# Kernel optimization log

Hardware: AMD Instinct MI355X
Metric: run time of the kernel (lower is better)

The kernel has to match this reference:

```python
import jax, jax.numpy as jnp
import numpy as np

EPS = 1e-6


def setup_inputs() -> dict:
    key = jax.random.key(0)
    k1, k2 = jax.random.split(key)
    B, Lq, Lk, D = 16, 1024, 1024, 512
    query = jax.random.normal(k1, (B, Lq, D), dtype=jnp.float32)
    context = jax.random.normal(k2, (B, Lk, D), dtype=jnp.float32)
    gamma = jnp.ones((D,), dtype=jnp.float32)
    beta = jnp.zeros((D,), dtype=jnp.float32)
    return {"query": query, "context": context, "gamma": gamma, "beta": beta}


def _layer_norm(x, gamma, beta):
    mean = jnp.mean(x, axis=-1, keepdims=True)
    var = jnp.var(x, axis=-1, keepdims=True)
    return gamma * (x - mean) * jax.lax.rsqrt(var + EPS) + beta


def reference(query, context, gamma, beta):
    # query: [B, Lq, D], context: [B, Lk, D]
    D = query.shape[-1]
    scale = 1.0 / np.sqrt(D).astype(np.float32)
    # additive-style tanh-activated scores: [B, Lq, Lk]
    score = jnp.tanh(jnp.einsum('bqd,bkd->bqk', query, context) * scale)
    attn = jax.nn.softmax(score, axis=2)
    # dropout is identity in eval/reference mode
    out = jnp.einsum('bqk,bkd->bqd', attn, context)
    out = _layer_norm(out + query, gamma, beta)
    return out
```

## Files before the change

kernel.cpp:

```cpp
#include <hip/hip_runtime.h>
#include <hip/hip_bf16.h>
#include <cstdint>

#define LQ 1024
#define LK 1024
#define DD 512
#define NB 16
#define QB 64
#define KB 32
#define NT (LK / KB)
#define CSTRIDE 1088
#define CSZ (32 * CSTRIDE)

typedef short bf16x8 __attribute__((ext_vector_type(8)));
typedef float f32x4 __attribute__((ext_vector_type(4)));

__device__ __forceinline__ uint16_t f2bf(float f) {
  uint32_t u = __builtin_bit_cast(uint32_t, f);
  u = (u + 0x7fffu + ((u >> 16) & 1u)) >> 16;
  return (uint16_t)u;
}

__device__ __forceinline__ void load_lds16(const void* g, void* l) {
  __builtin_amdgcn_global_load_lds(
      (const __attribute__((address_space(1))) uint32_t*)g,
      (__attribute__((address_space(3))) uint32_t*)l, 16, 0, 0);
}

__global__ __launch_bounds__(256) void prep_kernel(const float* __restrict__ c,
                                                   uint16_t* __restrict__ cb,
                                                   uint16_t* __restrict__ ct) {
  __shared__ float t[32][33];
  const int k0 = blockIdx.x * 32, d0 = blockIdx.y * 32, b = blockIdx.z;
  const float* src = c + (size_t)b * LK * DD;
  uint16_t* cbd = cb + (size_t)b * LK * DD;
  uint16_t* ctd = ct + (size_t)b * DD * LK;
  const int tx = threadIdx.x, ty = threadIdx.y;
  for (int j = 0; j < 4; ++j) {
    int k = ty + j * 8;
    float v = src[(size_t)(k0 + k) * DD + d0 + tx];
    t[k][tx] = v;
    cbd[(size_t)(k0 + k) * DD + d0 + tx] = f2bf(v);
  }
  __syncthreads();
  for (int j = 0; j < 4; ++j) {
    int d = ty + j * 8;
    ctd[(size_t)(d0 + d) * LK + k0 + tx] = f2bf(t[tx][d]);
  }
}

__global__ __launch_bounds__(512, 2) void attn_kernel(
    const uint16_t* __restrict__ Cb, const uint16_t* __restrict__ Ctb,
    const float* __restrict__ Qf, const float* __restrict__ gamma,
    const float* __restrict__ beta, float* __restrict__ out) {
  __shared__ uint4 cs4[2 * CSZ / 16];
  __shared__ uint4 cts4[2 * 32 * 1024 / 16];
  __shared__ char plds[64 * 80];
  __shared__ float denom_s[QB];
  __shared__ float rsum_s[QB], rsumsq_s[QB], mean_s[QB], rstd_s[QB];

  const int tid = threadIdx.x;
  const int w = tid >> 6, l = tid & 63, c = l & 15, g = l >> 4;
  const int orig = blockIdx.x;
  const int virt = ((orig & 7) << 5) | (orig >> 3);
  const int b = virt >> 4, qblk = virt & 15;
  const int q0 = qblk * QB;
  const int mt = w & 1, qt = w >> 1;
  const float scale = 0.044194173824159216f;

  if (tid < QB) { denom_s[tid] = 0.f; rsum_s[tid] = 0.f; rsumsq_s[tid] = 0.f; }

  bf16x8 qfrag[16];
  {
    const float* qrow = Qf + ((size_t)b * LQ + q0 + qt * 16 + c) * DD;
    for (int s = 0; s < 16; ++s) {
      float4 a0 = *(const float4*)(qrow + s * 32 + g * 8);
      float4 a1 = *(const float4*)(qrow + s * 32 + g * 8 + 4);
      ushort4 u0, u1;
      u0.x = f2bf(a0.x); u0.y = f2bf(a0.y); u0.z = f2bf(a0.z); u0.w = f2bf(a0.w);
      u1.x = f2bf(a1.x); u1.y = f2bf(a1.y); u1.z = f2bf(a1.z); u1.w = f2bf(a1.w);
      union { ushort4 u[2]; bf16x8 v; } pk;
      pk.u[0] = u0; pk.u[1] = u1;
      qfrag[s] = pk.v;
    }
  }

  const int kkA = mt * 16 + c;
  const int aoff = kkA * CSTRIDE + ((g ^ (kkA & 3)) * 16);

  f32x4 oacc[4][4];
  for (int i = 0; i < 4; ++i)
    for (int j = 0; j < 4; ++j) oacc[i][j] = (f32x4){0.f, 0.f, 0.f, 0.f};
  float dacc = 0.f;

  const char* cbyte = (const char*)Cb + (size_t)b * LK * DD * 2;
  const char* ctbyte = (const char*)Ctb + (size_t)b * DD * LK * 2;

  int csrcoff[4];
  for (int j = 0; j < 4; ++j) {
    int r = w * 4 + j;
    csrcoff[j] = r * 1024 + ((l * 16) ^ ((r & 3) << 4));
  }

  char* cs0 = (char*)cs4;
  char* cs1 = cs0 + CSZ;
  char* cts0 = (char*)cts4;
  char* cts1 = cts0 + 32 * 1024;
  const int pwoff = (qt * 16 + c) * 80 + (mt * 16 + g * 4) * 2;
  const int proff = c * 80 + g * 16;

  auto stageC = [&](char* dst, int kt2) {
    const char* s0 = cbyte + (size_t)kt2 * 32768;
    for (int j = 0; j < 4; ++j)
      load_lds16(s0 + csrcoff[j], dst + (w * 4 + j) * CSTRIDE);
  };
  auto stageCT = [&](char* dst, int kt2) {
    const int kk0 = kt2 * KB;
    for (int j = 0; j < 4; ++j) {
      int d0l = w * 64 + j * 16;
      int d = d0l + (l >> 2);
      const char* src =
          ctbyte + (size_t)d * 2048 + kk0 * 2 + (((l & 3) * 16) ^ ((d & 3) << 4));
      load_lds16(src, dst + d0l * 64);
    }
  };

  stageC(cs0, 0);
  stageCT(cts0, 0);
  __syncthreads();

  for (int kt = 0; kt < NT; ++kt) {
    const int cur = kt & 1;
    const char* csR = cur ? cs1 : cs0;
    const char* ctsR = cur ? cts1 : cts0;
    if (kt + 1 < NT) {
      stageC(cur ? cs0 : cs1, kt + 1);
      stageCT(cur ? cts0 : cts1, kt + 1);
    }
    f32x4 s0v = {0.f, 0.f, 0.f, 0.f}, s1v = {0.f, 0.f, 0.f, 0.f};
    f32x4 s2v = {0.f, 0.f, 0.f, 0.f}, s3v = {0.f, 0.f, 0.f, 0.f};
    {
      const char* ar = csR + aoff;
      for (int s = 0; s < 4; ++s) {
        bf16x8 a0 = *(const bf16x8*)(ar + s * 64);
        bf16x8 a1 = *(const bf16x8*)(ar + (s + 4) * 64);
        bf16x8 a2 = *(const bf16x8*)(ar + (s + 8) * 64);
        bf16x8 a3 = *(const bf16x8*)(ar + (s + 12) * 64);
        s0v = __builtin_amdgcn_mfma_f32_16x16x32_bf16(a0, qfrag[s], s0v, 0, 0, 0);
        s1v = __builtin_amdgcn_mfma_f32_16x16x32_bf16(a1, qfrag[s + 4], s1v, 0, 0, 0);
        s2v = __builtin_amdgcn_mfma_f32_16x16x32_bf16(a2, qfrag[s + 8], s2v, 0, 0, 0);
        s3v = __builtin_amdgcn_mfma_f32_16x16x32_bf16(a3, qfrag[s + 12], s3v, 0, 0, 0);
      }
    }
    {
      float pv[4];
      for (int i = 0; i < 4; ++i) {
        float sv = ((s0v[i] + s1v[i]) + (s2v[i] + s3v[i])) * scale;
        float e2 = __expf(sv * 2.f);
        float r = __builtin_amdgcn_rcpf(e2 + 1.f);
        float th = (e2 - 1.f) * r;
        float p = __expf(th);
        pv[i] = p;
        dacc += p;
      }
      uint2 pk;
      asm("v_cvt_pk_bf16_f32 %0, %1, %2" : "=v"(pk.x) : "v"(pv[0]), "v"(pv[1]));
      asm("v_cvt_pk_bf16_f32 %0, %1, %2" : "=v"(pk.y) : "v"(pv[2]), "v"(pv[3]));
      *(uint2*)(plds + pwoff) = pk;
    }
    asm volatile("s_waitcnt lgkmcnt(0)" ::: "memory");
    __builtin_amdgcn_s_barrier();
    __builtin_amdgcn_sched_barrier(0);

    {
      bf16x8 pa[4], pb[4];
      for (int q2 = 0; q2 < 4; ++q2)
        pa[q2] = *(const bf16x8*)(plds + proff + q2 * 1280);
      for (int nt = 0; nt < 4; ++nt) {
        int d = w * 64 + nt * 16 + c;
        pb[nt] = *(const bf16x8*)(ctsR + d * 64 + ((g * 16) ^ ((d & 3) << 4)));
      }
      for (int q2 = 0; q2 < 4; ++q2)
        for (int n2 = 0; n2 < 4; ++n2)
          oacc[q2][n2] =
              __builtin_amdgcn_mfma_f32_16x16x32_bf16(pa[q2], pb[n2], oacc[q2][n2], 0, 0, 0);
    }
    __syncthreads();
  }

  float dv = dacc;
  dv += __shfl_xor(dv, 16);
  dv += __shfl_xor(dv, 32);
  if (l < 16) atomicAdd(&denom_s[qt * 16 + l], dv);
  __syncthreads();

  const float* qsrc = Qf + ((size_t)b * LQ + q0) * DD;
  for (int q2 = 0; q2 < 4; ++q2)
    for (int i = 0; i < 4; ++i) {
      int row = q2 * 16 + g * 4 + i;
      float inv = 1.f / denom_s[row];
      for (int nt = 0; nt < 4; ++nt) {
        int d = w * 64 + nt * 16 + c;
        float o = oacc[q2][nt][i] * inv + qsrc[(size_t)row * DD + d];
        oacc[q2][nt][i] = o;
      }
    }
  for (int q2 = 0; q2 < 4; ++q2)
    for (int i = 0; i < 4; ++i) {
      float s1 = 0.f, s2 = 0.f;
      for (int nt = 0; nt < 4; ++nt) {
        float v = oacc[q2][nt][i];
        s1 += v;
        s2 += v * v;
      }
      s1 += __shfl_xor(s1, 1); s2 += __shfl_xor(s2, 1);
      s1 += __shfl_xor(s1, 2); s2 += __shfl_xor(s2, 2);
      s1 += __shfl_xor(s1, 4); s2 += __shfl_xor(s2, 4);
      s1 += __shfl_xor(s1, 8); s2 += __shfl_xor(s2, 8);
      if (c == 0) {
        int row = q2 * 16 + g * 4 + i;
        atomicAdd(&rsum_s[row], s1);
        atomicAdd(&rsumsq_s[row], s2);
      }
    }
  __syncthreads();
  if (tid < QB) {
    float m = rsum_s[tid] * (1.f / DD);
    float var = rsumsq_s[tid] * (1.f / DD) - m * m;
    mean_s[tid] = m;
    rstd_s[tid] = rsqrtf(fmaxf(var, 0.f) + 1e-6f);
  }
  __syncthreads();
  float* op = out + ((size_t)b * LQ + q0) * DD;
  for (int q2 = 0; q2 < 4; ++q2)
    for (int i = 0; i < 4; ++i) {
      int row = q2 * 16 + g * 4 + i;
      float m = mean_s[row], r = rstd_s[row];
      for (int nt = 0; nt < 4; ++nt) {
        int d = w * 64 + nt * 16 + c;
        op[(size_t)row * DD + d] = gamma[d] * ((oacc[q2][nt][i] - m) * r) + beta[d];
      }
    }
}

__global__ __launch_bounds__(256) void naive_kernel(const float* __restrict__ Q,
                                                    const float* __restrict__ C,
                                                    const float* __restrict__ gamma,
                                                    const float* __restrict__ beta,
                                                    float* __restrict__ out) {
  const int row = blockIdx.x;
  const int b = row >> 10;
  const int tid = threadIdx.x;
  __shared__ float qs[DD];
  __shared__ float ps[LK];
  __shared__ float ys[DD];
  __shared__ float red[256];
  const float* qp = Q + (size_t)row * DD;
  const float* cb = C + (size_t)b * LK * DD;
  for (int d = tid; d < DD; d += 256) qs[d] = qp[d];
  __syncthreads();
  for (int k = tid; k < LK; k += 256) {
    const float* cr = cb + (size_t)k * DD;
    float s = 0.f;
    for (int d = 0; d < DD; ++d) s += qs[d] * cr[d];
    s *= 0.044194173824159216f;
    float e2 = __expf(2.f * s);
    float th = (e2 - 1.f) / (e2 + 1.f);
    ps[k] = __expf(th);
  }
  __syncthreads();
  float dsum = 0.f;
  for (int k = tid; k < LK; k += 256) dsum += ps[k];
  red[tid] = dsum;
  __syncthreads();
  for (int off = 128; off; off >>= 1) {
    if (tid < off) red[tid] += red[tid + off];
    __syncthreads();
  }
  float inv = 1.f / red[0];
  __syncthreads();
  for (int d = tid; d < DD; d += 256) {
    float o = 0.f;
    for (int k = 0; k < LK; ++k) o += ps[k] * cb[(size_t)k * DD + d];
    ys[d] = o * inv + qs[d];
  }
  __syncthreads();
  float s1 = 0.f;
  for (int d = tid; d < DD; d += 256) s1 += ys[d];
  red[tid] = s1;
  __syncthreads();
  for (int off = 128; off; off >>= 1) {
    if (tid < off) red[tid] += red[tid + off];
    __syncthreads();
  }
  float mean = red[0] * (1.f / DD);
  __syncthreads();
  float s2 = 0.f;
  for (int d = tid; d < DD; d += 256) {
    float v = ys[d] - mean;
    s2 += v * v;
  }
  red[tid] = s2;
  __syncthreads();
  for (int off = 128; off; off >>= 1) {
    if (tid < off) red[tid] += red[tid + off];
    __syncthreads();
  }
  float rstd = rsqrtf(red[0] * (1.f / DD) + 1e-6f);
  for (int d = tid; d < DD; d += 256)
    out[(size_t)row * DD + d] = gamma[d] * ((ys[d] - mean) * rstd) + beta[d];
}

extern "C" void kernel_launch(void* const* d_in, const int* in_sizes, int n_in,
                              void* d_out, int out_size, void* d_ws, size_t ws_size,
                              hipStream_t stream) {
  const float* Qf = (const float*)d_in[0];
  const float* Cf = (const float*)d_in[1];
  const float* gamma = (const float*)d_in[2];
  const float* beta = (const float*)d_in[3];
  float* out = (float*)d_out;
  const size_t nelem = (size_t)NB * LK * DD;
  const size_t need = nelem * 2 * 2;
  if (ws_size >= need) {
    uint16_t* Cb = (uint16_t*)d_ws;
    uint16_t* Ctb = Cb + nelem;
    prep_kernel<<<dim3(LK / 32, DD / 32, NB), dim3(32, 8), 0, stream>>>(Cf, Cb, Ctb);
    attn_kernel<<<256, 512, 0, stream>>>(Cb, Ctb, Qf, gamma, beta, out);
  } else {
    naive_kernel<<<NB * LQ, 256, 0, stream>>>(Qf, Cf, gamma, beta, out);
  }
}
```

Measured before the change: 82.32 us.

## Split waves into score producers and PV consumers with warp specialization

Waves 0-3 now compute the QK scores and tanh-softmax numerators for two query tiles each and write them to shared memory. Waves 4-7 each hold a 64x128 output accumulator and run the P·V MFMAs plus the residual add and layernorm. Each group stages only its own operand (C for the producers, C transposed for the consumers). The aim is to overlap the two GEMM phases across wave groups and to cut redundant staging. The cost is higher register pressure in the consumer waves and lockstep barrier matching between the two branches.

```diff
diff --git a/kernel.cpp b/kernel.cpp
--- a/kernel.cpp
+++ b/kernel.cpp
@@ -65,182 +65,226 @@
   const int virt = ((orig & 7) << 5) | (orig >> 3);
   const int b = virt >> 4, qblk = virt & 15;
   const int q0 = qblk * QB;
-  const int mt = w & 1, qt = w >> 1;
   const float scale = 0.044194173824159216f;
 
   if (tid < QB) { denom_s[tid] = 0.f; rsum_s[tid] = 0.f; rsumsq_s[tid] = 0.f; }
-
-  bf16x8 qfrag[16];
-  {
-    const float* qrow = Qf + ((size_t)b * LQ + q0 + qt * 16 + c) * DD;
-    for (int s = 0; s < 16; ++s) {
-      float4 a0 = *(const float4*)(qrow + s * 32 + g * 8);
-      float4 a1 = *(const float4*)(qrow + s * 32 + g * 8 + 4);
-      ushort4 u0, u1;
-      u0.x = f2bf(a0.x); u0.y = f2bf(a0.y); u0.z = f2bf(a0.z); u0.w = f2bf(a0.w);
-      u1.x = f2bf(a1.x); u1.y = f2bf(a1.y); u1.z = f2bf(a1.z); u1.w = f2bf(a1.w);
-      union { ushort4 u[2]; bf16x8 v; } pk;
-      pk.u[0] = u0; pk.u[1] = u1;
-      qfrag[s] = pk.v;
-    }
-  }
-
-  const int kkA = mt * 16 + c;
-  const int aoff = kkA * CSTRIDE + ((g ^ (kkA & 3)) * 16);
-
-  f32x4 oacc[4][4];
-  for (int i = 0; i < 4; ++i)
-    for (int j = 0; j < 4; ++j) oacc[i][j] = (f32x4){0.f, 0.f, 0.f, 0.f};
-  float dacc = 0.f;
 
   const char* cbyte = (const char*)Cb + (size_t)b * LK * DD * 2;
   const char* ctbyte = (const char*)Ctb + (size_t)b * DD * LK * 2;
-
-  int csrcoff[4];
-  for (int j = 0; j < 4; ++j) {
-    int r = w * 4 + j;
-    csrcoff[j] = r * 1024 + ((l * 16) ^ ((r & 3) << 4));
-  }
-
   char* cs0 = (char*)cs4;
   char* cs1 = cs0 + CSZ;
   char* cts0 = (char*)cts4;
   char* cts1 = cts0 + 32 * 1024;
-  const int pwoff = (qt * 16 + c) * 80 + (mt * 16 + g * 4) * 2;
   const int proff = c * 80 + g * 16;
 
-  auto stageC = [&](char* dst, int kt2) {
-    const char* s0 = cbyte + (size_t)kt2 * 32768;
-    for (int j = 0; j < 4; ++j)
-      load_lds16(s0 + csrcoff[j], dst + (w * 4 + j) * CSTRIDE);
-  };
-  auto stageCT = [&](char* dst, int kt2) {
-    const int kk0 = kt2 * KB;
+  {
+    for (int j = 0; j < 4; ++j) {
+      int r = w * 4 + j;
+      load_lds16(cbyte + r * 1024 + ((l * 16) ^ ((r & 3) << 4)),
+                 cs0 + r * CSTRIDE);
+    }
     for (int j = 0; j < 4; ++j) {
       int d0l = w * 64 + j * 16;
       int d = d0l + (l >> 2);
-      const char* src =
-          ctbyte + (size_t)d * 2048 + kk0 * 2 + (((l & 3) * 16) ^ ((d & 3) << 4));
-      load_lds16(src, dst + d0l * 64);
-    }
-  };
-
-  stageC(cs0, 0);
-  stageCT(cts0, 0);
-  __syncthreads();
-
-  for (int kt = 0; kt < NT; ++kt) {
-    const int cur = kt & 1;
-    const char* csR = cur ? cs1 : cs0;
-    const char* ctsR = cur ? cts1 : cts0;
-    if (kt + 1 < NT) {
-      stageC(cur ? cs0 : cs1, kt + 1);
-      stageCT(cur ? cts0 : cts1, kt + 1);
-    }
-    f32x4 s0v = {0.f, 0.f, 0.f, 0.f}, s1v = {0.f, 0.f, 0.f, 0.f};
-    f32x4 s2v = {0.f, 0.f, 0.f, 0.f}, s3v = {0.f, 0.f, 0.f, 0.f};
+      load_lds16(ctbyte + (size_t)d * 2048 + (((l & 3) * 16) ^ ((d & 3) << 4)),
+                 cts0 + d0l * 64);
+    }
+  }
+  __syncthreads();
+
+  if (w < 4) {
+    const int mt = w & 1, qa = w >> 1, qb2 = qa + 2;
+    bf16x8 qfA[16], qfB[16];
     {
-      const char* ar = csR + aoff;
-      for (int s = 0; s < 4; ++s) {
-        bf16x8 a0 = *(const bf16x8*)(ar + s * 64);
-        bf16x8 a1 = *(const bf16x8*)(ar + (s + 4) * 64);
-        bf16x8 a2 = *(const bf16x8*)(ar + (s + 8) * 64);
-        bf16x8 a3 = *(const bf16x8*)(ar + (s + 12) * 64);
-        s0v = __builtin_amdgcn_mfma_f32_16x16x32_bf16(a0, qfrag[s], s0v, 0, 0, 0);
-        s1v = __builtin_amdgcn_mfma_f32_16x16x32_bf16(a1, qfrag[s + 4], s1v, 0, 0, 0);
-        s2v = __builtin_amdgcn_mfma_f32_16x16x32_bf16(a2, qfrag[s + 8], s2v, 0, 0, 0);
-        s3v = __builtin_amdgcn_mfma_f32_16x16x32_bf16(a3, qfrag[s + 12], s3v, 0, 0, 0);
-      }
-    }
-    {
-      float pv[4];
+      const float* ra = Qf + ((size_t)b * LQ + q0 + qa * 16 + c) * DD;
+      const float* rb = Qf + ((size_t)b * LQ + q0 + qb2 * 16 + c) * DD;
+      for (int s = 0; s < 16; ++s) {
+        float4 a0 = *(const float4*)(ra + s * 32 + g * 8);
+        float4 a1 = *(const float4*)(ra + s * 32 + g * 8 + 4);
+        ushort4 u0, u1;
+        u0.x = f2bf(a0.x); u0.y = f2bf(a0.y); u0.z = f2bf(a0.z); u0.w = f2bf(a0.w);
+        u1.x = f2bf(a1.x); u1.y = f2bf(a1.y); u1.z = f2bf(a1.z); u1.w = f2bf(a1.w);
+        union { ushort4 u[2]; bf16x8 v; } pk;
+        pk.u[0] = u0; pk.u[1] = u1;
+        qfA[s] = pk.v;
+        float4 b0 = *(const float4*)(rb + s * 32 + g * 8);
+        float4 b1 = *(const float4*)(rb + s * 32 + g * 8 + 4);
+        ushort4 v0, v1;
+        v0.x = f2bf(b0.x); v0.y = f2bf(b0.y); v0.z = f2bf(b0.z); v0.w = f2bf(b0.w);
+        v1.x = f2bf(b1.x); v1.y = f2bf(b1.y); v1.z = f2bf(b1.z); v1.w = f2bf(b1.w);
+        union { ushort4 u[2]; bf16x8 v; } pk2;
+        pk2.u[0] = v0; pk2.u[1] = v1;
+        qfB[s] = pk2.v;
+      }
+    }
+    const int kkA = mt * 16 + c;
+    const int aoff = kkA * CSTRIDE + ((g ^ (kkA & 3)) * 16);
+    int csoff[8];
+    for (int j = 0; j < 8; ++j) {
+      int r = w * 8 + j;
+      csoff[j] = r * 1024 + ((l * 16) ^ ((r & 3) << 4));
+    }
+    const int pwA = (qa * 16 + c) * 80 + (mt * 16 + g * 4) * 2;
+    const int pwB = (qb2 * 16 + c) * 80 + (mt * 16 + g * 4) * 2;
+    float dA = 0.f, dB = 0.f;
+
+    for (int kt = 0; kt < NT; ++kt) {
+      const int cur = kt & 1;
+      if (kt + 1 < NT) {
+        const char* s0 = cbyte + (size_t)(kt + 1) * 32768;
+        char* dst = cur ? cs0 : cs1;
+        for (int j = 0; j < 8; ++j)
+          load_lds16(s0 + csoff[j], dst + (w * 8 + j) * CSTRIDE);
+      }
+      f32x4 sA0 = {0,0,0,0}, sA1 = {0,0,0,0}, sA2 = {0,0,0,0}, sA3 = {0,0,0,0};
+      f32x4 sB0 = {0,0,0,0}, sB1 = {0,0,0,0}, sB2 = {0,0,0,0}, sB3 = {0,0,0,0};
+      {
+        const char* ar = (cur ? cs1 : cs0) + aoff;
+        for (int s = 0; s < 4; ++s) {
+          bf16x8 a0 = *(const bf16x8*)(ar + s * 64);
+          bf16x8 a1 = *(const bf16x8*)(ar + (s + 4) * 64);
+          bf16x8 a2 = *(const bf16x8*)(ar + (s + 8) * 64);
+          bf16x8 a3 = *(const bf16x8*)(ar + (s + 12) * 64);
+          sA0 = __builtin_amdgcn_mfma_f32_16x16x32_bf16(a0, qfA[s], sA0, 0, 0, 0);
+          sB0 = __builtin_amdgcn_mfma_f32_16x16x32_bf16(a0, qfB[s], sB0, 0, 0, 0);
+          sA1 = __builtin_amdgcn_mfma_f32_16x16x32_bf16(a1, qfA[s + 4], sA1, 0, 0, 0);
+          sB1 = __builtin_amdgcn_mfma_f32_16x16x32_bf16(a1, qfB[s + 4], sB1, 0, 0, 0);
+          sA2 = __builtin_amdgcn_mfma_f32_16x16x32_bf16(a2, qfA[s + 8], sA2, 0, 0, 0);
+          sB2 = __builtin_amdgcn_mfma_f32_16x16x32_bf16(a2, qfB[s + 8], sB2, 0, 0, 0);
+          sA3 = __builtin_amdgcn_mfma_f32_16x16x32_bf16(a3, qfA[s + 12], sA3, 0, 0, 0);
+          sB3 = __builtin_amdgcn_mfma_f32_16x16x32_bf16(a3, qfB[s + 12], sB3, 0, 0, 0);
+        }
+      }
+      {
+        float pvA[4], pvB[4];
+        for (int i = 0; i < 4; ++i) {
+          float sv = ((sA0[i] + sA1[i]) + (sA2[i] + sA3[i])) * scale;
+          float e2 = __expf(sv * 2.f);
+          float th = (e2 - 1.f) * __builtin_amdgcn_rcpf(e2 + 1.f);
+          float p = __expf(th);
+          pvA[i] = p;
+          dA += p;
+          float sw = ((sB0[i] + sB1[i]) + (sB2[i] + sB3[i])) * scale;
+          float f2 = __expf(sw * 2.f);
+          float tg = (f2 - 1.f) * __builtin_amdgcn_rcpf(f2 + 1.f);
+          float q = __expf(tg);
+          pvB[i] = q;
+          dB += q;
+        }
+        uint2 ka, kb;
+        asm("v_cvt_pk_bf16_f32 %0, %1, %2" : "=v"(ka.x) : "v"(pvA[0]), "v"(pvA[1]));
+        asm("v_cvt_pk_bf16_f32 %0, %1, %2" : "=v"(ka.y) : "v"(pvA[2]), "v"(pvA[3]));
+        asm("v_cvt_pk_bf16_f32 %0, %1, %2" : "=v"(kb.x) : "v"(pvB[0]), "v"(pvB[1]));
+        asm("v_cvt_pk_bf16_f32 %0, %1, %2" : "=v"(kb.y) : "v"(pvB[2]), "v"(pvB[3]));
+        *(uint2*)(plds + pwA) = ka;
+        *(uint2*)(plds + pwB) = kb;
+      }
+      asm volatile("s_waitcnt lgkmcnt(0)" ::: "memory");
+      __builtin_amdgcn_s_barrier();
+      __builtin_amdgcn_sched_barrier(0);
+      __syncthreads();
+    }
+    float dv = dA;
+    dv += __shfl_xor(dv, 16);
+    dv += __shfl_xor(dv, 32);
+    if (l < 16) atomicAdd(&denom_s[qa * 16 + l], dv);
+    float dw = dB;
+    dw += __shfl_xor(dw, 16);
+    dw += __shfl_xor(dw, 32);
+    if (l < 16) atomicAdd(&denom_s[qb2 * 16 + l], dw);
+    __syncthreads();
+    __syncthreads();
+    if (tid < QB) {
+      float m = rsum_s[tid] * (1.f / DD);
+      float var = rsumsq_s[tid] * (1.f / DD) - m * m;
+      mean_s[tid] = m;
+      rstd_s[tid] = rsqrtf(fmaxf(var, 0.f) + 1e-6f);
+    }
+    __syncthreads();
+  } else {
+    const int cw = w - 4;
+    f32x4 oacc[4][8];
+    for (int i = 0; i < 4; ++i)
+      for (int j = 0; j < 8; ++j) oacc[i][j] = (f32x4){0.f, 0.f, 0.f, 0.f};
+    int ctsrc[8], ctdst[8], pboff[8];
+    for (int j = 0; j < 8; ++j) {
+      int d0l = cw * 128 + j * 16;
+      int d = d0l + (l >> 2);
+      ctsrc[j] = d * 2048 + (((l & 3) * 16) ^ ((d & 3) << 4));
+      ctdst[j] = d0l * 64;
+      int dp = cw * 128 + j * 16 + c;
+      pboff[j] = dp * 64 + ((g * 16) ^ ((dp & 3) << 4));
+    }
+
+    for (int kt = 0; kt < NT; ++kt) {
+      const int cur = kt & 1;
+      const char* ctsR = cur ? cts1 : cts0;
+      if (kt + 1 < NT) {
+        const int kk0 = (kt + 1) * KB;
+        char* dst = cur ? cts0 : cts1;
+        for (int j = 0; j < 8; ++j)
+          load_lds16(ctbyte + (size_t)ctsrc[j] + kk0 * 2, dst + ctdst[j]);
+      }
+      bf16x8 pb[8];
+      for (int nt = 0; nt < 8; ++nt)
+        pb[nt] = *(const bf16x8*)(ctsR + pboff[nt]);
+      __builtin_amdgcn_s_barrier();
+      __builtin_amdgcn_sched_barrier(0);
+      {
+        bf16x8 pa[4];
+        for (int q2 = 0; q2 < 4; ++q2)
+          pa[q2] = *(const bf16x8*)(plds + proff + q2 * 1280);
+        for (int q2 = 0; q2 < 4; ++q2)
+          for (int n2 = 0; n2 < 8; ++n2)
+            oacc[q2][n2] =
+                __builtin_amdgcn_mfma_f32_16x16x32_bf16(pa[q2], pb[n2], oacc[q2][n2], 0, 0, 0);
+      }
+      __syncthreads();
+    }
+    __syncthreads();
+
+    const float* qsrc = Qf + ((size_t)b * LQ + q0) * DD;
+    for (int q2 = 0; q2 < 4; ++q2)
       for (int i = 0; i < 4; ++i) {
-        float sv = ((s0v[i] + s1v[i]) + (s2v[i] + s3v[i])) * scale;
-        float e2 = __expf(sv * 2.f);
-        float r = __builtin_amdgcn_rcpf(e2 + 1.f);
-        float th = (e2 - 1.f) * r;
-        float p = __expf(th);
-        pv[i] = p;
-        dacc += p;
-      }
-      uint2 pk;
-      asm("v_cvt_pk_bf16_f32 %0, %1, %2" : "=v"(pk.x) : "v"(pv[0]), "v"(pv[1]));
-      asm("v_cvt_pk_bf16_f32 %0, %1, %2" : "=v"(pk.y) : "v"(pv[2]), "v"(pv[3]));
-      *(uint2*)(plds + pwoff) = pk;
-    }
-    asm volatile("s_waitcnt lgkmcnt(0)" ::: "memory");
-    __builtin_amdgcn_s_barrier();
-    __builtin_amdgcn_sched_barrier(0);
-
-    {
-      bf16x8 pa[4], pb[4];
-      for (int q2 = 0; q2 < 4; ++q2)
-        pa[q2] = *(const bf16x8*)(plds + proff + q2 * 1280);
-      for (int nt = 0; nt < 4; ++nt) {
-        int d = w * 64 + nt * 16 + c;
-        pb[nt] = *(const bf16x8*)(ctsR + d * 64 + ((g * 16) ^ ((d & 3) << 4)));
-      }
-      for (int q2 = 0; q2 < 4; ++q2)
-        for (int n2 = 0; n2 < 4; ++n2)
-          oacc[q2][n2] =
-              __builtin_amdgcn_mfma_f32_16x16x32_bf16(pa[q2], pb[n2], oacc[q2][n2], 0, 0, 0);
-    }
-    __syncthreads();
-  }
-
-  float dv = dacc;
-  dv += __shfl_xor(dv, 16);
-  dv += __shfl_xor(dv, 32);
-  if (l < 16) atomicAdd(&denom_s[qt * 16 + l], dv);
-  __syncthreads();
-
-  const float* qsrc = Qf + ((size_t)b * LQ + q0) * DD;
-  for (int q2 = 0; q2 < 4; ++q2)
-    for (int i = 0; i < 4; ++i) {
-      int row = q2 * 16 + g * 4 + i;
-      float inv = 1.f / denom_s[row];
-      for (int nt = 0; nt < 4; ++nt) {
-        int d = w * 64 + nt * 16 + c;
-        float o = oacc[q2][nt][i] * inv + qsrc[(size_t)row * DD + d];
-        oacc[q2][nt][i] = o;
-      }
-    }
-  for (int q2 = 0; q2 < 4; ++q2)
-    for (int i = 0; i < 4; ++i) {
-      float s1 = 0.f, s2 = 0.f;
-      for (int nt = 0; nt < 4; ++nt) {
-        float v = oacc[q2][nt][i];
-        s1 += v;
-        s2 += v * v;
-      }
-      s1 += __shfl_xor(s1, 1); s2 += __shfl_xor(s2, 1);
-      s1 += __shfl_xor(s1, 2); s2 += __shfl_xor(s2, 2);
-      s1 += __shfl_xor(s1, 4); s2 += __shfl_xor(s2, 4);
-      s1 += __shfl_xor(s1, 8); s2 += __shfl_xor(s2, 8);
-      if (c == 0) {
         int row = q2 * 16 + g * 4 + i;
-        atomicAdd(&rsum_s[row], s1);
-        atomicAdd(&rsumsq_s[row], s2);
-      }
-    }
-  __syncthreads();
-  if (tid < QB) {
-    float m = rsum_s[tid] * (1.f / DD);
-    float var = rsumsq_s[tid] * (1.f / DD) - m * m;
-    mean_s[tid] = m;
-    rstd_s[tid] = rsqrtf(fmaxf(var, 0.f) + 1e-6f);
-  }
-  __syncthreads();
-  float* op = out + ((size_t)b * LQ + q0) * DD;
-  for (int q2 = 0; q2 < 4; ++q2)
-    for (int i = 0; i < 4; ++i) {
-      int row = q2 * 16 + g * 4 + i;
-      float m = mean_s[row], r = rstd_s[row];
-      for (int nt = 0; nt < 4; ++nt) {
-        int d = w * 64 + nt * 16 + c;
-        op[(size_t)row * DD + d] = gamma[d] * ((oacc[q2][nt][i] - m) * r) + beta[d];
-      }
-    }
+        float inv = 1.f / denom_s[row];
+        for (int nt = 0; nt < 8; ++nt) {
+          int d = cw * 128 + nt * 16 + c;
+          float o = oacc[q2][nt][i] * inv + qsrc[(size_t)row * DD + d];
+          oacc[q2][nt][i] = o;
+        }
+      }
+    for (int q2 = 0; q2 < 4; ++q2)
+      for (int i = 0; i < 4; ++i) {
+        float s1 = 0.f, s2 = 0.f;
+        for (int nt = 0; nt < 8; ++nt) {
+          float v = oacc[q2][nt][i];
+          s1 += v;
+          s2 += v * v;
+        }
+        s1 += __shfl_xor(s1, 1); s2 += __shfl_xor(s2, 1);
+        s1 += __shfl_xor(s1, 2); s2 += __shfl_xor(s2, 2);
+        s1 += __shfl_xor(s1, 4); s2 += __shfl_xor(s2, 4);
+        s1 += __shfl_xor(s1, 8); s2 += __shfl_xor(s2, 8);
+        if (c == 0) {
+          int row = q2 * 16 + g * 4 + i;
+          atomicAdd(&rsum_s[row], s1);
+          atomicAdd(&rsumsq_s[row], s2);
+        }
+      }
+    __syncthreads();
+    __syncthreads();
+    float* op = out + ((size_t)b * LQ + q0) * DD;
+    for (int q2 = 0; q2 < 4; ++q2)
+      for (int i = 0; i < 4; ++i) {
+        int row = q2 * 16 + g * 4 + i;
+        float m = mean_s[row], r = rstd_s[row];
+        for (int nt = 0; nt < 8; ++nt) {
+          int d = cw * 128 + nt * 16 + c;
+          op[(size_t)row * DD + d] = gamma[d] * ((oacc[q2][nt][i] - m) * r) + beta[d];
+        }
+      }
+  }
 }
 
 __global__ __launch_bounds__(256) void naive_kernel(const float* __restrict__ Q,
```

Result: slower. 89.25 us (+8.4%).
